# Performance work log

Hardware: AMD Instinct MI355X
Metric: run time of the kernel (lower is better)

Reference implementation:

```python
import jax, jax.numpy as jnp
import numpy as np

N_NODES = 50000
N_EDGES = 800000
D_IN = 128
D_HID = 128
D_OUT = 1
N_GRAPHS = 64
NEG_SLOPE = 0.2


def gat_layer(x, src, dst, W, a_src, a_dst, b, n_nodes):
    # x: [N, d_in] -> h: [N, d_hid]
    h = x @ W
    alpha_s = h @ a_src  # [N]
    alpha_d = h @ a_dst  # [N]
    e = jax.nn.leaky_relu(alpha_s[src] + alpha_d[dst], NEG_SLOPE)  # [E]
    # segment softmax over destination neighborhoods
    m = jax.ops.segment_max(e, dst, num_segments=n_nodes)
    ex = jnp.exp(e - m[dst])
    denom = jax.ops.segment_sum(ex, dst, num_segments=n_nodes)
    alpha = ex / (denom[dst] + 1e-16)  # [E]
    out = jax.ops.segment_sum(h[src] * alpha[:, None], dst, num_segments=n_nodes)
    return out + b


def setup_inputs() -> dict:
    key = jax.random.key(0)
    ks = jax.random.split(key, 16)
    x = jax.random.normal(ks[0], (N_NODES, D_IN), dtype=jnp.float32)
    edge_index = jax.random.randint(ks[1], (2, N_EDGES), 0, N_NODES, dtype=jnp.int32)
    batch = jnp.sort(jax.random.randint(ks[2], (N_NODES,), 0, N_GRAPHS, dtype=jnp.int32))
    inp = {"x": x, "edge_index": edge_index, "batch": batch}
    dims = [(D_IN, D_HID), (D_HID, D_HID), (D_HID, D_HID), (D_HID, D_HID)]
    for i, (di, dh) in enumerate(dims, 1):
        kk = jax.random.split(ks[2 + i], 4)
        s = 1.0 / np.sqrt(di)
        inp[f"W{i}"] = jax.random.uniform(kk[0], (di, dh), jnp.float32, -s, s)
        inp[f"a_src{i}"] = jax.random.uniform(kk[1], (dh,), jnp.float32, -s, s)
        inp[f"a_dst{i}"] = jax.random.uniform(kk[2], (dh,), jnp.float32, -s, s)
        inp[f"b{i}"] = jnp.zeros((dh,), jnp.float32)
    s = 1.0 / np.sqrt(D_HID)
    inp["fcW"] = jax.random.uniform(ks[10], (D_HID, D_OUT), jnp.float32, -s, s)
    inp["fcb"] = jnp.zeros((D_OUT,), jnp.float32)
    return inp


def reference(x, edge_index, batch,
              W1, a_src1, a_dst1, b1,
              W2, a_src2, a_dst2, b2,
              W3, a_src3, a_dst3, b3,
              W4, a_src4, a_dst4, b4,
              fcW, fcb):
    n = x.shape[0]
    loops = jnp.arange(n, dtype=edge_index.dtype)
    src = jnp.concatenate([edge_index[0], loops])  # add self-loops (PyG default)
    dst = jnp.concatenate([edge_index[1], loops])
    h = jax.nn.relu(gat_layer(x, src, dst, W1, a_src1, a_dst1, b1, n))
    h = jax.nn.relu(gat_layer(h, src, dst, W2, a_src2, a_dst2, b2, n))
    h = jax.nn.relu(gat_layer(h, src, dst, W3, a_src3, a_dst3, b3, n))
    h = jax.nn.relu(gat_layer(h, src, dst, W4, a_src4, a_dst4, b4, n))
    # global mean pool over graphs
    sums = jax.ops.segment_sum(h, batch, num_segments=N_GRAPHS)
    counts = jax.ops.segment_sum(jnp.ones((n,), h.dtype), batch, num_segments=N_GRAPHS)
    pooled = sums / jnp.maximum(counts, 1.0)[:, None]
    return pooled @ fcW + fcb
```

## Files before the change

### kernel.cpp

```cpp
#include <hip/hip_runtime.h>

#define N_NODES 50000
#define N_EDGES 800000
#define E_TOT (N_EDGES + N_NODES)
#define D 128
#define N_GRAPHS 64
#define NEG_SLOPE 0.2f
#define MAXDEG 256
#define SCAN_BLK 1024
#define SCAN_GRID ((N_NODES + SCAN_BLK - 1) / SCAN_BLK)

typedef _Float16 f16x8 __attribute__((ext_vector_type(8)));
typedef _Float16 f16x4 __attribute__((ext_vector_type(4)));
typedef _Float16 f16x2 __attribute__((ext_vector_type(2)));
typedef float f32x4 __attribute__((ext_vector_type(4)));

__device__ __forceinline__ float wave_max(float v) {
  #pragma unroll
  for (int off = 32; off > 0; off >>= 1) v = fmaxf(v, __shfl_xor(v, off));
  return v;
}
__device__ __forceinline__ float wave_sum(float v) {
  #pragma unroll
  for (int off = 32; off > 0; off >>= 1) v += __shfl_xor(v, off);
  return v;
}

__global__ void k_count(const int* __restrict__ ei, int* __restrict__ cnt,
                        unsigned short* __restrict__ rank) {
  int e = blockIdx.x * blockDim.x + threadIdx.x;
  if (e >= E_TOT) return;
  int dst = (e < N_EDGES) ? ei[N_EDGES + e] : (e - N_EDGES);
  rank[e] = (unsigned short)atomicAdd(&cnt[dst], 1);
}

__global__ __launch_bounds__(SCAN_BLK) void k_scan1(const int* __restrict__ cnt,
                                                    int* __restrict__ rowptr,
                                                    int* __restrict__ partial) {
  __shared__ int sm[SCAN_BLK];
  int i = blockIdx.x * SCAN_BLK + threadIdx.x;
  int v = (i < N_NODES) ? cnt[i] : 0;
  sm[threadIdx.x] = v;
  __syncthreads();
  #pragma unroll
  for (int off = 1; off < SCAN_BLK; off <<= 1) {
    int t = (threadIdx.x >= off) ? sm[threadIdx.x - off] : 0;
    __syncthreads();
    sm[threadIdx.x] += t;
    __syncthreads();
  }
  if (i < N_NODES) rowptr[i + 1] = sm[threadIdx.x];
  if (threadIdx.x == SCAN_BLK - 1) partial[blockIdx.x] = sm[threadIdx.x];
}

__global__ void k_scan2(int* __restrict__ partial) {
  int lane = threadIdx.x;
  int v = (lane < SCAN_GRID) ? partial[lane] : 0;
  #pragma unroll
  for (int off = 1; off < 64; off <<= 1) {
    int t = __shfl_up(v, off);
    if (lane >= off) v += t;
  }
  if (lane < SCAN_GRID) partial[lane] = v;
}

__global__ __launch_bounds__(SCAN_BLK) void k_scan3(int* __restrict__ rowptr,
                                                    const int* __restrict__ partial) {
  int i = blockIdx.x * SCAN_BLK + threadIdx.x;
  if (i == 0) rowptr[0] = 0;
  if (i < N_NODES && blockIdx.x > 0) rowptr[i + 1] += partial[blockIdx.x - 1];
}

struct WPtrs {
  const float* w[4];
  _Float16* h[4];
  _Float16* l[4];
};
__global__ __launch_bounds__(256) void k_wconv_all(WPtrs p) {
  int layer = blockIdx.x >> 6;
  int e = (blockIdx.x & 63) * 256 + threadIdx.x;
  int k = e >> 7, n = e & 127;
  float v = p.w[layer][e];
  _Float16 h = (_Float16)v;
  _Float16 lo = (_Float16)(v - (float)h);
  int idx = (n >> 4) * 2048 + (k >> 3) * 128 + (n & 15) * 8 + (k & 7);
  p.h[layer][idx] = h;
  p.l[layer][idx] = lo;
}

template <int MODE>
__global__ __launch_bounds__(256) void k_gemm_mfma(const void* __restrict__ Xv,
                                                   const _Float16* __restrict__ Whf,
                                                   const _Float16* __restrict__ Wlf,
                                                   _Float16* __restrict__ Hh,
                                                   const float* __restrict__ asrc,
                                                   const float* __restrict__ adst,
                                                   float* __restrict__ alpha_s,
                                                   float* __restrict__ alpha_d,
                                                   const int* __restrict__ ei,
                                                   const int* __restrict__ rowptr,
                                                   const unsigned short* __restrict__ rank,
                                                   unsigned short* __restrict__ col) {
  __shared__ __align__(16) _Float16 AhL[8192];
  __shared__ __align__(16) _Float16 AlL[MODE ? 8192 : 1];
  const int tid = threadIdx.x;
  const int l = tid & 63;
  const int w = tid >> 6;
  const int rowbase = blockIdx.x * 64;

  #pragma unroll
  for (int p = 0; p < 4; ++p) {
    int row = p * 16 + (tid >> 4);
    int k0 = (tid & 15) * 8;
    int grow = rowbase + row;
    int idx = (((row >> 4) * 16 + (k0 >> 3)) * 16 + (row & 15)) * 8;
    if (MODE) {
      const float* X = (const float*)Xv;
      float xv[8];
      if (grow < N_NODES) {
        float4 f0 = *reinterpret_cast<const float4*>(&X[(size_t)grow * D + k0]);
        float4 f1 = *reinterpret_cast<const float4*>(&X[(size_t)grow * D + k0 + 4]);
        xv[0] = f0.x; xv[1] = f0.y; xv[2] = f0.z; xv[3] = f0.w;
        xv[4] = f1.x; xv[5] = f1.y; xv[6] = f1.z; xv[7] = f1.w;
      } else {
        #pragma unroll
        for (int j = 0; j < 8; ++j) xv[j] = 0.f;
      }
      f16x8 ah, al;
      #pragma unroll
      for (int j = 0; j < 8; ++j) {
        ah[j] = (_Float16)xv[j];
        al[j] = (_Float16)(xv[j] - (float)ah[j]);
      }
      *reinterpret_cast<f16x8*>(&AhL[idx]) = ah;
      *reinterpret_cast<f16x8*>(&AlL[idx]) = al;
    } else {
      const _Float16* X = (const _Float16*)Xv;
      f16x8 ah = {0, 0, 0, 0, 0, 0, 0, 0};
      if (grow < N_NODES)
        ah = *reinterpret_cast<const f16x8*>(&X[(size_t)grow * D + k0]);
      *reinterpret_cast<f16x8*>(&AhL[idx]) = ah;
    }
  }
  __syncthreads();

  f32x4 acc[8];
  #pragma unroll
  for (int cc = 0; cc < 8; ++cc) acc[cc] = (f32x4){0.f, 0.f, 0.f, 0.f};

  #pragma unroll
  for (int kt = 0; kt < 4; ++kt) {
    int aidx = w * 2048 + kt * 512 + l * 8;
    f16x8 ah = *reinterpret_cast<const f16x8*>(&AhL[aidx]);
    f16x8 al;
    if (MODE) al = *reinterpret_cast<const f16x8*>(&AlL[aidx]);
    #pragma unroll
    for (int cc = 0; cc < 8; ++cc) {
      int bidx = cc * 2048 + kt * 512 + l * 8;
      f16x8 bh = *reinterpret_cast<const f16x8*>(&Whf[bidx]);
      f16x8 bl = *reinterpret_cast<const f16x8*>(&Wlf[bidx]);
      acc[cc] = __builtin_amdgcn_mfma_f32_16x16x32_f16(ah, bh, acc[cc], 0, 0, 0);
      acc[cc] = __builtin_amdgcn_mfma_f32_16x16x32_f16(ah, bl, acc[cc], 0, 0, 0);
      if (MODE)
        acc[cc] = __builtin_amdgcn_mfma_f32_16x16x32_f16(al, bh, acc[cc], 0, 0, 0);
    }
  }

  const int myn = l & 15;
  const int rg4 = l >> 4;
  float asv[8], adv[8];
  #pragma unroll
  for (int cc = 0; cc < 8; ++cc) {
    asv[cc] = asrc[cc * 16 + myn];
    adv[cc] = adst[cc * 16 + myn];
  }
  #pragma unroll
  for (int reg = 0; reg < 4; ++reg) {
    int grow = rowbase + w * 16 + rg4 * 4 + reg;
    float ps = 0.f, pd = 0.f;
    #pragma unroll
    for (int cc = 0; cc < 8; ++cc) {
      float v = acc[cc][reg];
      ps = fmaf(v, asv[cc], ps);
      pd = fmaf(v, adv[cc], pd);
      if (grow < N_NODES) Hh[(size_t)grow * D + cc * 16 + myn] = (_Float16)v;
    }
    #pragma unroll
    for (int off = 1; off < 16; off <<= 1) {
      ps += __shfl_xor(ps, off);
      pd += __shfl_xor(pd, off);
    }
    if (grow < N_NODES && myn == 0) {
      alpha_s[grow] = ps;
      alpha_d[grow] = pd;
    }
  }

  if (MODE) {
    int stride = gridDim.x * blockDim.x;
    for (int e = blockIdx.x * blockDim.x + tid; e < E_TOT; e += stride) {
      int src, dst;
      if (e < N_EDGES) { src = ei[e]; dst = ei[N_EDGES + e]; }
      else { src = e - N_EDGES; dst = src; }
      col[rowptr[dst] + rank[e]] = (unsigned short)src;
    }
  }
}

template <int FINAL>
__global__ __launch_bounds__(256) void k_agg(const _Float16* __restrict__ Hh,
                                             const int* __restrict__ rowptr,
                                             const unsigned short* __restrict__ col,
                                             const float* __restrict__ alpha_s,
                                             const float* __restrict__ alpha_d,
                                             const float* __restrict__ bias,
                                             _Float16* __restrict__ Out,
                                             const float* __restrict__ fcW,
                                             float* __restrict__ ynode) {
  __shared__ float wls[4][MAXDEG];
  __shared__ unsigned cls[4][MAXDEG];
  int wid = threadIdx.x >> 6;
  int lane = threadIdx.x & 63;
  int node = blockIdx.x * 4 + wid;
  if (node >= N_NODES) return;
  int start = rowptr[node], end = rowptr[node + 1];
  int deg = end - start;
  float ad = alpha_d[node];

  float earr[4];
  float m = -1e30f;
  #pragma unroll
  for (int k = 0; k < 4; ++k) {
    int j0 = lane + k * 64;
    earr[k] = -1e30f;
    if (j0 < deg) {
      int s = col[start + j0];
      float e = alpha_s[s] + ad;
      e = e >= 0.f ? e : NEG_SLOPE * e;
      cls[wid][j0] = (unsigned)s << 8;
      earr[k] = e;
    }
  }
  m = fmaxf(fmaxf(earr[0], earr[1]), fmaxf(earr[2], earr[3]));
  for (int j0 = MAXDEG + lane; j0 < deg; j0 += 64) {
    int s = col[start + j0];
    float e = alpha_s[s] + ad;
    e = e >= 0.f ? e : NEG_SLOPE * e;
    m = fmaxf(m, e);
  }
  m = wave_max(m);

  float dsum = 0.f;
  #pragma unroll
  for (int k = 0; k < 4; ++k) {
    int j0 = lane + k * 64;
    if (j0 < deg) {
      float w = expf(earr[k] - m);
      wls[wid][j0] = w;
      dsum += w;
    }
  }
  for (int j0 = MAXDEG + lane; j0 < deg; j0 += 64) {
    int s = col[start + j0];
    float e = alpha_s[s] + ad;
    e = e >= 0.f ? e : NEG_SLOPE * e;
    dsum += expf(e - m);
  }
  dsum = wave_sum(dsum);
  float inv = 1.f / (dsum + 1e-16f);

  int degc = deg < MAXDEG ? deg : MAXDEG;
  int degc8 = (degc + 7) & ~7;
  for (int j0 = degc + lane; j0 < degc8; j0 += 64) {
    cls[wid][j0] = 0;
    wls[wid][j0] = 0.f;
  }

  const unsigned fo8 = (unsigned)(lane & 31) * 8;
  const int e2 = lane >> 5;
  const char* hbase = (const char*)Hh;
  f32x4 acc4 = {0.f, 0.f, 0.f, 0.f};
  for (int jj = 0; jj < degc8; jj += 8) {
    unsigned offs[4];
    float w4[4];
    f16x4 hv[4];
    #pragma unroll
    for (int u = 0; u < 4; ++u) {
      int idx = jj + u * 2 + e2;
      offs[u] = cls[wid][idx] + fo8;
      w4[u] = wls[wid][idx];
      hv[u] = *reinterpret_cast<const f16x4*>(hbase + offs[u]);
    }
    #pragma unroll
    for (int u = 0; u < 4; ++u) {
      acc4.x = fmaf((float)hv[u][0], w4[u], acc4.x);
      acc4.y = fmaf((float)hv[u][1], w4[u], acc4.y);
      acc4.z = fmaf((float)hv[u][2], w4[u], acc4.z);
      acc4.w = fmaf((float)hv[u][3], w4[u], acc4.w);
    }
  }
  for (int jj = MAXDEG; jj < deg; jj += 2) {
    int idx = jj + e2;
    bool ok = idx < deg;
    int s = ok ? (int)col[start + idx] : 0;
    float e = alpha_s[s] + ad;
    e = e >= 0.f ? e : NEG_SLOPE * e;
    float w = ok ? expf(e - m) : 0.f;
    f16x4 hv = *reinterpret_cast<const f16x4*>(hbase + ((unsigned)s << 8) + fo8);
    acc4.x = fmaf((float)hv[0], w, acc4.x);
    acc4.y = fmaf((float)hv[1], w, acc4.y);
    acc4.z = fmaf((float)hv[2], w, acc4.z);
    acc4.w = fmaf((float)hv[3], w, acc4.w);
  }
  acc4.x += __shfl_xor(acc4.x, 32);
  acc4.y += __shfl_xor(acc4.y, 32);
  acc4.z += __shfl_xor(acc4.z, 32);
  acc4.w += __shfl_xor(acc4.w, 32);

  if (FINAL) {
    float y = 0.f;
    if (e2 == 0) {
      f32x4 bv = *reinterpret_cast<const f32x4*>(&bias[(lane & 31) * 4]);
      f32x4 wv = *reinterpret_cast<const f32x4*>(&fcW[(lane & 31) * 4]);
      float o0 = fmaxf(fmaf(acc4.x, inv, bv.x), 0.f);
      float o1 = fmaxf(fmaf(acc4.y, inv, bv.y), 0.f);
      float o2 = fmaxf(fmaf(acc4.z, inv, bv.z), 0.f);
      float o3 = fmaxf(fmaf(acc4.w, inv, bv.w), 0.f);
      y = o0 * wv.x + o1 * wv.y + o2 * wv.z + o3 * wv.w;
    }
    y = wave_sum(y);
    if (lane == 0) ynode[node] = y;
  } else {
    if (e2 == 0) {
      f32x4 bv = *reinterpret_cast<const f32x4*>(&bias[(lane & 31) * 4]);
      f16x4 oh;
      oh[0] = (_Float16)fmaxf(fmaf(acc4.x, inv, bv.x), 0.f);
      oh[1] = (_Float16)fmaxf(fmaf(acc4.y, inv, bv.y), 0.f);
      oh[2] = (_Float16)fmaxf(fmaf(acc4.z, inv, bv.z), 0.f);
      oh[3] = (_Float16)fmaxf(fmaf(acc4.w, inv, bv.w), 0.f);
      *reinterpret_cast<f16x4*>((char*)Out + (size_t)node * 256 + fo8) = oh;
    }
  }
}

__global__ __launch_bounds__(256) void k_final(const float* __restrict__ ynode,
                                               const int* __restrict__ batch,
                                               const float* __restrict__ fcb,
                                               float* __restrict__ out) {
  __shared__ float sm[256];
  int b = blockIdx.x;
  int tid = threadIdx.x;
  int lo = 0, hi = N_NODES;
  while (lo < hi) { int mid = (lo + hi) >> 1; if (batch[mid] < b) lo = mid + 1; else hi = mid; }
  int s0 = lo;
  lo = 0; hi = N_NODES;
  while (lo < hi) { int mid = (lo + hi) >> 1; if (batch[mid] < b + 1) lo = mid + 1; else hi = mid; }
  int s1 = lo;
  float sum = 0.f;
  for (int n = s0 + tid; n < s1; n += 256) sum += ynode[n];
  sm[tid] = sum;
  __syncthreads();
  #pragma unroll
  for (int off = 128; off > 0; off >>= 1) {
    if (tid < off) sm[tid] += sm[tid + off];
    __syncthreads();
  }
  if (tid == 0) out[b] = sm[0] / fmaxf((float)(s1 - s0), 1.f) + fcb[0];
}

extern "C" void kernel_launch(void* const* d_in, const int* in_sizes, int n_in,
                              void* d_out, int out_size, void* d_ws, size_t ws_size,
                              hipStream_t stream) {
  const float* x = (const float*)d_in[0];
  const int* ei = (const int*)d_in[1];
  const int* batch = (const int*)d_in[2];
  const float* W[4]   = {(const float*)d_in[3], (const float*)d_in[7],
                         (const float*)d_in[11], (const float*)d_in[15]};
  const float* asr[4] = {(const float*)d_in[4], (const float*)d_in[8],
                         (const float*)d_in[12], (const float*)d_in[16]};
  const float* adt[4] = {(const float*)d_in[5], (const float*)d_in[9],
                         (const float*)d_in[13], (const float*)d_in[17]};
  const float* bs[4]  = {(const float*)d_in[6], (const float*)d_in[10],
                         (const float*)d_in[14], (const float*)d_in[18]};
  const float* fcW = (const float*)d_in[19];
  const float* fcb = (const float*)d_in[20];
  float* out = (float*)d_out;

  char* ws = (char*)d_ws;
  size_t off = 0;
  _Float16* Hh  = (_Float16*)(ws + off); off += (size_t)N_NODES * D * 2;
  _Float16* hBh = (_Float16*)(ws + off); off += (size_t)N_NODES * D * 2;
  float* alpha_s = (float*)(ws + off); off += (size_t)N_NODES * 4;
  float* alpha_d = (float*)(ws + off); off += (size_t)N_NODES * 4;
  int* cnt  = (int*)(ws + off); off += (size_t)N_NODES * 4;
  int* rowptr = (int*)(ws + off); off += (size_t)(N_NODES + 1) * 4 + 12;
  unsigned short* col = (unsigned short*)(ws + off); off += ((size_t)E_TOT * 2 + 15) & ~15ull;
  unsigned short* rank = (unsigned short*)(ws + off); off += ((size_t)E_TOT * 2 + 15) & ~15ull;
  float* ynode = (float*)(ws + off); off += (size_t)N_NODES * 4;
  int* partial = (int*)(ws + off); off += ((size_t)SCAN_GRID * 4 + 15) & ~15ull;
  _Float16* Whf[4];
  _Float16* Wlf[4];
  for (int lyr = 0; lyr < 4; ++lyr) {
    Whf[lyr] = (_Float16*)(ws + off); off += (size_t)D * D * 2;
    Wlf[lyr] = (_Float16*)(ws + off); off += (size_t)D * D * 2;
  }
  (void)ws_size; (void)in_sizes; (void)n_in; (void)out_size;

  hipMemsetAsync(cnt, 0, (size_t)N_NODES * 4, stream);
  WPtrs wp;
  for (int lyr = 0; lyr < 4; ++lyr) { wp.w[lyr] = W[lyr]; wp.h[lyr] = Whf[lyr]; wp.l[lyr] = Wlf[lyr]; }
  k_wconv_all<<<256, 256, 0, stream>>>(wp);
  int eb = (E_TOT + 255) / 256;
  k_count<<<eb, 256, 0, stream>>>(ei, cnt, rank);
  k_scan1<<<SCAN_GRID, SCAN_BLK, 0, stream>>>(cnt, rowptr, partial);
  k_scan2<<<1, 64, 0, stream>>>(partial);
  k_scan3<<<SCAN_GRID, SCAN_BLK, 0, stream>>>(rowptr, partial);

  int gb = (N_NODES + 63) / 64;
  k_gemm_mfma<1><<<gb, 256, 0, stream>>>(x, Whf[0], Wlf[0], Hh, asr[0], adt[0],
                                         alpha_s, alpha_d, ei, rowptr, rank, col);
  k_agg<0><<<(N_NODES + 3) / 4, 256, 0, stream>>>(Hh, rowptr, col, alpha_s, alpha_d,
                                                  bs[0], hBh, nullptr, nullptr);
  for (int l = 1; l < 4; ++l) {
    k_gemm_mfma<0><<<gb, 256, 0, stream>>>(hBh, Whf[l], Wlf[l], Hh, asr[l], adt[l],
                                           alpha_s, alpha_d, nullptr, nullptr,
                                           nullptr, nullptr);
    if (l < 3) {
      k_agg<0><<<(N_NODES + 3) / 4, 256, 0, stream>>>(Hh, rowptr, col, alpha_s, alpha_d,
                                                      bs[l], hBh, nullptr, nullptr);
    } else {
      k_agg<1><<<(N_NODES + 3) / 4, 256, 0, stream>>>(Hh, rowptr, col, alpha_s, alpha_d,
                                                      bs[l], nullptr, fcW, ynode);
    }
  }
  k_final<<<N_GRAPHS, 256, 0, stream>>>(ynode, batch, fcb, out);
}
```

Before: 291.1 us.

## Compute softmax with 16-lane groups and aggregate four nodes per wave

The aggregation kernel now assigns 16 nodes per block. Each 16-lane quarter-wave computes the edge scores, max and softmax denominator for one node, instead of a full 64-lane wave working on a single node of average degree about 17. Each wave then loops over its four nodes for the feature gather, reading per-node state staged in shared memory. MAXDEG is halved to 128 to keep shared memory in bounds, and nodes above that degree take the slower recompute path. The aim is to stop wasting most lanes in the softmax phase and to cut block count, at the cost of serialising the gather over four nodes per wave.

```diff
diff --git a/kernel.cpp b/kernel.cpp
--- a/kernel.cpp
+++ b/kernel.cpp
@@ -6,20 +6,14 @@
 #define D 128
 #define N_GRAPHS 64
 #define NEG_SLOPE 0.2f
-#define MAXDEG 256
+#define MAXDEG 128
 #define SCAN_BLK 1024
 #define SCAN_GRID ((N_NODES + SCAN_BLK - 1) / SCAN_BLK)
 
 typedef _Float16 f16x8 __attribute__((ext_vector_type(8)));
 typedef _Float16 f16x4 __attribute__((ext_vector_type(4)));
-typedef _Float16 f16x2 __attribute__((ext_vector_type(2)));
 typedef float f32x4 __attribute__((ext_vector_type(4)));
 
-__device__ __forceinline__ float wave_max(float v) {
-  #pragma unroll
-  for (int off = 32; off > 0; off >>= 1) v = fmaxf(v, __shfl_xor(v, off));
-  return v;
-}
 __device__ __forceinline__ float wave_sum(float v) {
   #pragma unroll
   for (int off = 32; off > 0; off >>= 1) v += __shfl_xor(v, off);
@@ -217,128 +211,149 @@
                                              _Float16* __restrict__ Out,
                                              const float* __restrict__ fcW,
                                              float* __restrict__ ynode) {
-  __shared__ float wls[4][MAXDEG];
-  __shared__ unsigned cls[4][MAXDEG];
-  int wid = threadIdx.x >> 6;
-  int lane = threadIdx.x & 63;
-  int node = blockIdx.x * 4 + wid;
-  if (node >= N_NODES) return;
-  int start = rowptr[node], end = rowptr[node + 1];
-  int deg = end - start;
-  float ad = alpha_d[node];
-
-  float earr[4];
-  float m = -1e30f;
-  #pragma unroll
-  for (int k = 0; k < 4; ++k) {
-    int j0 = lane + k * 64;
-    earr[k] = -1e30f;
-    if (j0 < deg) {
-      int s = col[start + j0];
+  __shared__ float wls[16][MAXDEG];
+  __shared__ unsigned cls[16][MAXDEG];
+  __shared__ float sinv[16], smax[16];
+  __shared__ int sstart[16], sdeg[16];
+  const int tid = threadIdx.x;
+  const int wid = tid >> 6;
+  const int lane = tid & 63;
+  const int sub = lane >> 4;
+  const int t = lane & 15;
+  const int slot = wid * 4 + sub;
+  const int node = blockIdx.x * 16 + slot;
+
+  if (node < N_NODES) {
+    int start = rowptr[node];
+    int deg = rowptr[node + 1] - start;
+    float ad = alpha_d[node];
+    int degc = deg < MAXDEG ? deg : MAXDEG;
+    float m = -1e30f;
+    for (int j = t; j < degc; j += 16) {
+      int s = col[start + j];
       float e = alpha_s[s] + ad;
       e = e >= 0.f ? e : NEG_SLOPE * e;
-      cls[wid][j0] = (unsigned)s << 8;
-      earr[k] = e;
-    }
-  }
-  m = fmaxf(fmaxf(earr[0], earr[1]), fmaxf(earr[2], earr[3]));
-  for (int j0 = MAXDEG + lane; j0 < deg; j0 += 64) {
-    int s = col[start + j0];
-    float e = alpha_s[s] + ad;
-    e = e >= 0.f ? e : NEG_SLOPE * e;
-    m = fmaxf(m, e);
-  }
-  m = wave_max(m);
-
-  float dsum = 0.f;
-  #pragma unroll
-  for (int k = 0; k < 4; ++k) {
-    int j0 = lane + k * 64;
-    if (j0 < deg) {
-      float w = expf(earr[k] - m);
-      wls[wid][j0] = w;
+      cls[slot][j] = (unsigned)s << 8;
+      wls[slot][j] = e;
+      m = fmaxf(m, e);
+    }
+    for (int j = MAXDEG + t; j < deg; j += 16) {
+      int s = col[start + j];
+      float e = alpha_s[s] + ad;
+      e = e >= 0.f ? e : NEG_SLOPE * e;
+      m = fmaxf(m, e);
+    }
+    #pragma unroll
+    for (int off = 1; off < 16; off <<= 1) m = fmaxf(m, __shfl_xor(m, off));
+
+    float dsum = 0.f;
+    for (int j = t; j < degc; j += 16) {
+      float w = expf(wls[slot][j] - m);
+      wls[slot][j] = w;
       dsum += w;
     }
-  }
-  for (int j0 = MAXDEG + lane; j0 < deg; j0 += 64) {
-    int s = col[start + j0];
-    float e = alpha_s[s] + ad;
-    e = e >= 0.f ? e : NEG_SLOPE * e;
-    dsum += expf(e - m);
-  }
-  dsum = wave_sum(dsum);
-  float inv = 1.f / (dsum + 1e-16f);
-
-  int degc = deg < MAXDEG ? deg : MAXDEG;
-  int degc8 = (degc + 7) & ~7;
-  for (int j0 = degc + lane; j0 < degc8; j0 += 64) {
-    cls[wid][j0] = 0;
-    wls[wid][j0] = 0.f;
+    for (int j = MAXDEG + t; j < deg; j += 16) {
+      int s = col[start + j];
+      float e = alpha_s[s] + ad;
+      e = e >= 0.f ? e : NEG_SLOPE * e;
+      dsum += expf(e - m);
+    }
+    #pragma unroll
+    for (int off = 1; off < 16; off <<= 1) dsum += __shfl_xor(dsum, off);
+
+    int degc8 = (degc + 7) & ~7;
+    for (int j = degc + t; j < degc8; j += 16) {
+      cls[slot][j] = 0;
+      wls[slot][j] = 0.f;
+    }
+    if (t == 0) {
+      sinv[slot] = 1.f / (dsum + 1e-16f);
+      smax[slot] = m;
+      sstart[slot] = start;
+      sdeg[slot] = deg;
+    }
+  } else if (t == 0) {
+    sinv[slot] = 0.f; smax[slot] = 0.f; sstart[slot] = 0; sdeg[slot] = 0;
   }
 
   const unsigned fo8 = (unsigned)(lane & 31) * 8;
   const int e2 = lane >> 5;
   const char* hbase = (const char*)Hh;
-  f32x4 acc4 = {0.f, 0.f, 0.f, 0.f};
-  for (int jj = 0; jj < degc8; jj += 8) {
-    unsigned offs[4];
-    float w4[4];
-    f16x4 hv[4];
-    #pragma unroll
-    for (int u = 0; u < 4; ++u) {
-      int idx = jj + u * 2 + e2;
-      offs[u] = cls[wid][idx] + fo8;
-      w4[u] = wls[wid][idx];
-      hv[u] = *reinterpret_cast<const f16x4*>(hbase + offs[u]);
-    }
-    #pragma unroll
-    for (int u = 0; u < 4; ++u) {
-      acc4.x = fmaf((float)hv[u][0], w4[u], acc4.x);
-      acc4.y = fmaf((float)hv[u][1], w4[u], acc4.y);
-      acc4.z = fmaf((float)hv[u][2], w4[u], acc4.z);
-      acc4.w = fmaf((float)hv[u][3], w4[u], acc4.w);
-    }
-  }
-  for (int jj = MAXDEG; jj < deg; jj += 2) {
-    int idx = jj + e2;
-    bool ok = idx < deg;
-    int s = ok ? (int)col[start + idx] : 0;
-    float e = alpha_s[s] + ad;
-    e = e >= 0.f ? e : NEG_SLOPE * e;
-    float w = ok ? expf(e - m) : 0.f;
-    f16x4 hv = *reinterpret_cast<const f16x4*>(hbase + ((unsigned)s << 8) + fo8);
-    acc4.x = fmaf((float)hv[0], w, acc4.x);
-    acc4.y = fmaf((float)hv[1], w, acc4.y);
-    acc4.z = fmaf((float)hv[2], w, acc4.z);
-    acc4.w = fmaf((float)hv[3], w, acc4.w);
-  }
-  acc4.x += __shfl_xor(acc4.x, 32);
-  acc4.y += __shfl_xor(acc4.y, 32);
-  acc4.z += __shfl_xor(acc4.z, 32);
-  acc4.w += __shfl_xor(acc4.w, 32);
-
-  if (FINAL) {
-    float y = 0.f;
-    if (e2 == 0) {
-      f32x4 bv = *reinterpret_cast<const f32x4*>(&bias[(lane & 31) * 4]);
-      f32x4 wv = *reinterpret_cast<const f32x4*>(&fcW[(lane & 31) * 4]);
-      float o0 = fmaxf(fmaf(acc4.x, inv, bv.x), 0.f);
-      float o1 = fmaxf(fmaf(acc4.y, inv, bv.y), 0.f);
-      float o2 = fmaxf(fmaf(acc4.z, inv, bv.z), 0.f);
-      float o3 = fmaxf(fmaf(acc4.w, inv, bv.w), 0.f);
-      y = o0 * wv.x + o1 * wv.y + o2 * wv.z + o3 * wv.w;
-    }
-    y = wave_sum(y);
-    if (lane == 0) ynode[node] = y;
-  } else {
-    if (e2 == 0) {
-      f32x4 bv = *reinterpret_cast<const f32x4*>(&bias[(lane & 31) * 4]);
-      f16x4 oh;
-      oh[0] = (_Float16)fmaxf(fmaf(acc4.x, inv, bv.x), 0.f);
-      oh[1] = (_Float16)fmaxf(fmaf(acc4.y, inv, bv.y), 0.f);
-      oh[2] = (_Float16)fmaxf(fmaf(acc4.z, inv, bv.z), 0.f);
-      oh[3] = (_Float16)fmaxf(fmaf(acc4.w, inv, bv.w), 0.f);
-      *reinterpret_cast<f16x4*>((char*)Out + (size_t)node * 256 + fo8) = oh;
+  #pragma unroll
+  for (int n = 0; n < 4; ++n) {
+    const int ns = wid * 4 + n;
+    const int nnode = blockIdx.x * 16 + ns;
+    if (nnode >= N_NODES) continue;
+    const int ndeg = sdeg[ns];
+    const float ninv = sinv[ns];
+    int degc = ndeg < MAXDEG ? ndeg : MAXDEG;
+    int degc8 = (degc + 7) & ~7;
+    f32x4 acc4 = {0.f, 0.f, 0.f, 0.f};
+    for (int jj = 0; jj < degc8; jj += 8) {
+      unsigned offs[4];
+      float w4[4];
+      f16x4 hv[4];
+      #pragma unroll
+      for (int u = 0; u < 4; ++u) {
+        int idx = jj + u * 2 + e2;
+        offs[u] = cls[ns][idx] + fo8;
+        w4[u] = wls[ns][idx];
+        hv[u] = *reinterpret_cast<const f16x4*>(hbase + offs[u]);
+      }
+      #pragma unroll
+      for (int u = 0; u < 4; ++u) {
+        acc4.x = fmaf((float)hv[u][0], w4[u], acc4.x);
+        acc4.y = fmaf((float)hv[u][1], w4[u], acc4.y);
+        acc4.z = fmaf((float)hv[u][2], w4[u], acc4.z);
+        acc4.w = fmaf((float)hv[u][3], w4[u], acc4.w);
+      }
+    }
+    if (ndeg > MAXDEG) {
+      const int nstart = sstart[ns];
+      const float nm = smax[ns];
+      const float nad = alpha_d[nnode];
+      for (int jj = MAXDEG; jj < ndeg; jj += 2) {
+        int idx = jj + e2;
+        bool ok = idx < ndeg;
+        int s = ok ? (int)col[nstart + idx] : 0;
+        float e = alpha_s[s] + nad;
+        e = e >= 0.f ? e : NEG_SLOPE * e;
+        float w = ok ? expf(e - nm) : 0.f;
+        f16x4 hv = *reinterpret_cast<const f16x4*>(hbase + ((unsigned)s << 8) + fo8);
+        acc4.x = fmaf((float)hv[0], w, acc4.x);
+        acc4.y = fmaf((float)hv[1], w, acc4.y);
+        acc4.z = fmaf((float)hv[2], w, acc4.z);
+        acc4.w = fmaf((float)hv[3], w, acc4.w);
+      }
+    }
+    acc4.x += __shfl_xor(acc4.x, 32);
+    acc4.y += __shfl_xor(acc4.y, 32);
+    acc4.z += __shfl_xor(acc4.z, 32);
+    acc4.w += __shfl_xor(acc4.w, 32);
+
+    if (FINAL) {
+      float y = 0.f;
+      if (e2 == 0) {
+        f32x4 bv = *reinterpret_cast<const f32x4*>(&bias[(lane & 31) * 4]);
+        f32x4 wv = *reinterpret_cast<const f32x4*>(&fcW[(lane & 31) * 4]);
+        float o0 = fmaxf(fmaf(acc4.x, ninv, bv.x), 0.f);
+        float o1 = fmaxf(fmaf(acc4.y, ninv, bv.y), 0.f);
+        float o2 = fmaxf(fmaf(acc4.z, ninv, bv.z), 0.f);
+        float o3 = fmaxf(fmaf(acc4.w, ninv, bv.w), 0.f);
+        y = o0 * wv.x + o1 * wv.y + o2 * wv.z + o3 * wv.w;
+      }
+      y = wave_sum(y);
+      if (lane == 0) ynode[nnode] = y;
+    } else {
+      if (e2 == 0) {
+        f32x4 bv = *reinterpret_cast<const f32x4*>(&bias[(lane & 31) * 4]);
+        f16x4 oh;
+        oh[0] = (_Float16)fmaxf(fmaf(acc4.x, ninv, bv.x), 0.f);
+        oh[1] = (_Float16)fmaxf(fmaf(acc4.y, ninv, bv.y), 0.f);
+        oh[2] = (_Float16)fmaxf(fmaf(acc4.z, ninv, bv.z), 0.f);
+        oh[3] = (_Float16)fmaxf(fmaf(acc4.w, ninv, bv.w), 0.f);
+        *reinterpret_cast<f16x4*>((char*)Out + (size_t)nnode * 256 + fo8) = oh;
+      }
     }
   }
 }
@@ -417,20 +432,21 @@
   k_scan3<<<SCAN_GRID, SCAN_BLK, 0, stream>>>(rowptr, partial);
 
   int gb = (N_NODES + 63) / 64;
+  int ab = (N_NODES + 15) / 16;
   k_gemm_mfma<1><<<gb, 256, 0, stream>>>(x, Whf[0], Wlf[0], Hh, asr[0], adt[0],
                                          alpha_s, alpha_d, ei, rowptr, rank, col);
-  k_agg<0><<<(N_NODES + 3) / 4, 256, 0, stream>>>(Hh, rowptr, col, alpha_s, alpha_d,
-                                                  bs[0], hBh, nullptr, nullptr);
+  k_agg<0><<<ab, 256, 0, stream>>>(Hh, rowptr, col, alpha_s, alpha_d,
+                                   bs[0], hBh, nullptr, nullptr);
   for (int l = 1; l < 4; ++l) {
     k_gemm_mfma<0><<<gb, 256, 0, stream>>>(hBh, Whf[l], Wlf[l], Hh, asr[l], adt[l],
                                            alpha_s, alpha_d, nullptr, nullptr,
                                            nullptr, nullptr);
     if (l < 3) {
-      k_agg<0><<<(N_NODES + 3) / 4, 256, 0, stream>>>(Hh, rowptr, col, alpha_s, alpha_d,
-                                                      bs[l], hBh, nullptr, nullptr);
+      k_agg<0><<<ab, 256, 0, stream>>>(Hh, rowptr, col, alpha_s, alpha_d,
+                                       bs[l], hBh, nullptr, nullptr);
     } else {
-      k_agg<1><<<(N_NODES + 3) / 4, 256, 0, stream>>>(Hh, rowptr, col, alpha_s, alpha_d,
-                                                      bs[l], nullptr, fcW, ynode);
+      k_agg<1><<<ab, 256, 0, stream>>>(Hh, rowptr, col, alpha_s, alpha_d,
+                                       bs[l], nullptr, fcW, ynode);
     }
   }
   k_final<<<N_GRAPHS, 256, 0, stream>>>(ynode, batch, fcb, out);
```

New measurement: 274.9 us. -5.6%, faster.
